# Performance work log

Hardware: AMD Instinct MI355X
Metric: run time of the kernel (lower is better)

Reference implementation:

```python
import jax, jax.numpy as jnp
import numpy as np

N = 50000          # total nodes
E = 800000         # edges (avg degree 16)
IN = 128           # in_feat
HID = 64           # hidden per head
HEADS = (4, 4, 1)
NEG_SLOPE = 0.2    # DGL GATConv leaky_relu default


def setup_inputs() -> dict:
    key = jax.random.key(0)
    ks = jax.random.split(key, 16)

    def w(k, shape, fan_in):
        return jax.random.normal(k, shape, jnp.float32) / np.float32(np.sqrt(fan_in))

    inp = {
        "feat": jax.random.normal(ks[0], (N, IN), jnp.float32),
        "src": jax.random.randint(ks[1], (E,), 0, N, jnp.int32),
        "dst": jax.random.randint(ks[2], (E,), 0, N, jnp.int32),
    }
    dims = [(IN, HEADS[0]), (HID * HEADS[0], HEADS[1]), (HID * HEADS[1], HEADS[2])]
    j = 3
    for i, (din, h) in enumerate(dims, 1):
        inp[f"W{i}"] = w(ks[j], (din, h * HID), din); j += 1
        inp[f"al{i}"] = w(ks[j], (h, HID), HID); j += 1
        inp[f"ar{i}"] = w(ks[j], (h, HID), HID); j += 1
        inp[f"b{i}"] = jnp.zeros((h * HID,), jnp.float32)
    return inp


def gat_layer(x, W, al, ar, b, src, dst, n_heads):
    # DGL GATConv: linear -> per-node attn logits -> edge leaky_relu ->
    # per-dst segment softmax -> weighted scatter-sum -> + bias
    h = (x @ W).reshape(N, n_heads, HID)                     # [N,H,D]
    el = jnp.einsum("nhd,hd->nh", h, al)                     # [N,H]
    er = jnp.einsum("nhd,hd->nh", h, ar)                     # [N,H]
    e = jax.nn.leaky_relu(el[src] + er[dst], NEG_SLOPE)      # [E,H]
    m = jax.ops.segment_max(e, dst, num_segments=N)          # [N,H]
    m = jnp.where(jnp.isfinite(m), m, 0.0)                   # empty segments -> -inf
    ex = jnp.exp(e - m[dst])                                 # [E,H]
    s = jax.ops.segment_sum(ex, dst, num_segments=N)         # [N,H]
    alpha = ex / s[dst]                                      # [E,H]
    msg = h[src] * alpha[:, :, None]                         # [E,H,D]
    out = jax.ops.segment_sum(msg, dst, num_segments=N)      # [N,H,D]
    return out + b.reshape(1, n_heads, HID)


def reference(feat, src, dst, W1, al1, ar1, b1, W2, al2, ar2, b2, W3, al3, ar3, b3):
    h = jax.nn.elu(gat_layer(feat, W1, al1, ar1, b1, src, dst, HEADS[0]))
    h = h.reshape(N, HEADS[0] * HID)                         # flatten heads
    h = jax.nn.elu(gat_layer(h, W2, al2, ar2, b2, src, dst, HEADS[1]))
    h = h.reshape(N, HEADS[1] * HID)
    h = gat_layer(h, W3, al3, ar3, b3, src, dst, HEADS[2])   # no activation
    return h.mean(axis=1)                                    # [N, HID]
```

## Files before the change

kernel.cpp:

```cpp
#include <hip/hip_runtime.h>
#include <math.h>

#define HID 64
#define NSLOPE 0.2f
#define SB 512
#define EXCAP 256

typedef __attribute__((ext_vector_type(8))) short short8v;
typedef __attribute__((ext_vector_type(4))) float float4v;

__device__ inline unsigned short f2bf(float x) {
  unsigned u = __float_as_uint(x);
  u += 0x7fffu + ((u >> 16) & 1u);
  return (unsigned short)(u >> 16);
}
__device__ inline float bf2f(unsigned short h) {
  return __uint_as_float(((unsigned)h) << 16);
}
__device__ inline float bflo(unsigned u) { return __uint_as_float(u << 16); }
__device__ inline float bfhi(unsigned u) { return __uint_as_float(u & 0xffff0000u); }

__global__ __launch_bounds__(256) void k_split(const float* __restrict__ x,
    unsigned short* __restrict__ hi, unsigned short* __restrict__ lo, int n) {
  int i = blockIdx.x * 256 + threadIdx.x;
  if (i < n) {
    float v = x[i];
    unsigned short h = f2bf(v);
    hi[i] = h;
    lo[i] = f2bf(v - bf2f(h));
  }
}

__global__ __launch_bounds__(256) void k_wsplit(const float* __restrict__ W,
    unsigned short* __restrict__ Whi, unsigned short* __restrict__ Wlo, int K, int N) {
  int i = blockIdx.x * 256 + threadIdx.x;
  if (i < N * K) {
    int n = i / K, k = i - n * K;
    float v = W[(size_t)k * N + n];
    unsigned short h = f2bf(v);
    Whi[i] = h;
    Wlo[i] = f2bf(v - bf2f(h));
  }
}

__global__ __launch_bounds__(256) void gemm_split(
    const unsigned short* __restrict__ Ahi, const unsigned short* __restrict__ Alo,
    const unsigned short* __restrict__ Bhi, const unsigned short* __restrict__ Blo,
    float* __restrict__ C, unsigned short* __restrict__ Gp, int M, int Nc, int K, int H) {
  __shared__ __align__(16) unsigned short AsHi[128 * 40];
  __shared__ __align__(16) unsigned short AsLo[128 * 40];
  __shared__ __align__(16) unsigned short BsHi[128 * 40];
  __shared__ __align__(16) unsigned short BsLo[128 * 40];
  const int tid = threadIdx.x;
  const int lane = tid & 63, wid = tid >> 6;
  const int wr = wid >> 1, wc = wid & 1;
  const int row0 = blockIdx.y * 128;
  const int col0 = blockIdx.x * 128;
  float4v acc[4][4];
  #pragma unroll
  for (int mi = 0; mi < 4; ++mi)
    #pragma unroll
    for (int ni = 0; ni < 4; ++ni)
      acc[mi][ni] = (float4v){0.f, 0.f, 0.f, 0.f};

  const int sr = tid >> 2;
  const int sc8 = (tid & 3) * 8;
  const int lr = lane & 15, lk = (lane >> 4) * 8;

  for (int k0 = 0; k0 < K; k0 += 32) {
    #pragma unroll
    for (int half = 0; half < 2; ++half) {
      int row = sr + half * 64;
      int arow = row0 + row; if (arow > M - 1) arow = M - 1;
      int brow = col0 + row; if (brow > Nc - 1) brow = Nc - 1;
      *(short8v*)&AsHi[row * 40 + sc8] = *(const short8v*)&Ahi[(size_t)arow * K + k0 + sc8];
      *(short8v*)&AsLo[row * 40 + sc8] = *(const short8v*)&Alo[(size_t)arow * K + k0 + sc8];
      *(short8v*)&BsHi[row * 40 + sc8] = *(const short8v*)&Bhi[(size_t)brow * K + k0 + sc8];
      *(short8v*)&BsLo[row * 40 + sc8] = *(const short8v*)&Blo[(size_t)brow * K + k0 + sc8];
    }
    __syncthreads();
    short8v ah[4], alv[4], bh[4], bl[4];
    #pragma unroll
    for (int mi = 0; mi < 4; ++mi) {
      int r = wr * 64 + mi * 16 + lr;
      ah[mi]  = *(const short8v*)&AsHi[r * 40 + lk];
      alv[mi] = *(const short8v*)&AsLo[r * 40 + lk];
    }
    #pragma unroll
    for (int ni = 0; ni < 4; ++ni) {
      int r = wc * 64 + ni * 16 + lr;
      bh[ni] = *(const short8v*)&BsHi[r * 40 + lk];
      bl[ni] = *(const short8v*)&BsLo[r * 40 + lk];
    }
    #pragma unroll
    for (int mi = 0; mi < 4; ++mi)
      #pragma unroll
      for (int ni = 0; ni < 4; ++ni) {
        acc[mi][ni] = __builtin_amdgcn_mfma_f32_16x16x32_bf16(ah[mi], bh[ni], acc[mi][ni], 0, 0, 0);
        acc[mi][ni] = __builtin_amdgcn_mfma_f32_16x16x32_bf16(ah[mi], bl[ni], acc[mi][ni], 0, 0, 0);
        acc[mi][ni] = __builtin_amdgcn_mfma_f32_16x16x32_bf16(alv[mi], bh[ni], acc[mi][ni], 0, 0, 0);
      }
    __syncthreads();
  }
  #pragma unroll
  for (int mi = 0; mi < 4; ++mi) {
    int rbase = row0 + wr * 64 + mi * 16 + (lane >> 4) * 4;
    #pragma unroll
    for (int ni = 0; ni < 4; ++ni) {
      int cc = col0 + wc * 64 + ni * 16 + (lane & 15);
      if (cc < Nc) {
        int gcol = (cc & 63) * H + (cc >> 6);
        #pragma unroll
        for (int q = 0; q < 4; ++q) {
          int rr = rbase + q;
          if (rr < M) {
            float v = acc[mi][ni][q];
            C[(size_t)rr * Nc + cc] = v;
            Gp[(size_t)rr * Nc + gcol] = f2bf(v);
          }
        }
      }
    }
  }
}

__global__ __launch_bounds__(256) void elr_kernel(const float* __restrict__ h,
    const float* __restrict__ al, const float* __restrict__ ar,
    float* __restrict__ el, float* __restrict__ er, int H, int N) {
  int n = blockIdx.x * 4 + (threadIdx.x >> 6);
  int lane = threadIdx.x & 63;
  if (n >= N) return;
  const float* hr = h + (size_t)n * H * HID;
  for (int hh = 0; hh < H; ++hh) {
    float v = hr[hh * HID + lane];
    float a = v * al[hh * HID + lane];
    float b = v * ar[hh * HID + lane];
    #pragma unroll
    for (int o = 32; o > 0; o >>= 1) { a += __shfl_xor(a, o); b += __shfl_xor(b, o); }
    if (lane == 0) { el[n * H + hh] = a; er[n * H + hh] = b; }
  }
}

__global__ void k_count(const int* __restrict__ dst, int* __restrict__ deg, int E) {
  int e = blockIdx.x * blockDim.x + threadIdx.x;
  if (e < E) atomicAdd(&deg[dst[e]], 1);
}
__global__ __launch_bounds__(SB) void k_blocksums(const int* __restrict__ deg,
                                                  int* __restrict__ bsums, int n) {
  __shared__ int s[SB];
  int t = threadIdx.x, i = blockIdx.x * SB + t;
  s[t] = (i < n) ? deg[i] : 0;
  __syncthreads();
  for (int o = SB >> 1; o > 0; o >>= 1) { if (t < o) s[t] += s[t + o]; __syncthreads(); }
  if (t == 0) bsums[blockIdx.x] = s[0];
}
__global__ __launch_bounds__(SB) void k_scancarry(const int* __restrict__ bsums,
                                                   int* __restrict__ carry, int nb) {
  __shared__ int s[SB];
  int t = threadIdx.x;
  int v = (t < nb) ? bsums[t] : 0;
  s[t] = v; __syncthreads();
  for (int o = 1; o < SB; o <<= 1) {
    int u = (t >= o) ? s[t - o] : 0;
    __syncthreads(); s[t] += u; __syncthreads();
  }
  if (t < nb) carry[t] = s[t] - v;
}
__global__ __launch_bounds__(SB) void k_offsets(const int* __restrict__ deg,
    const int* __restrict__ carry, int* __restrict__ offs, int n, int E) {
  __shared__ int s[SB];
  int t = threadIdx.x, i = blockIdx.x * SB + t;
  int v = (i < n) ? deg[i] : 0;
  s[t] = v; __syncthreads();
  for (int o = 1; o < SB; o <<= 1) {
    int u = (t >= o) ? s[t - o] : 0;
    __syncthreads(); s[t] += u; __syncthreads();
  }
  if (i < n) offs[i] = carry[blockIdx.x] + s[t] - v;
  if (i == n) offs[n] = E;
}
__global__ void k_fill(const int* __restrict__ src, const int* __restrict__ dst,
                       const int* __restrict__ offs, int* __restrict__ cursor,
                       int* __restrict__ esrc, int E) {
  int e = blockIdx.x * blockDim.x + threadIdx.x;
  if (e < E) {
    int d = dst[e];
    int slot = offs[d] + atomicAdd(&cursor[d], 1);
    esrc[slot] = src[e];
  }
}

template<int H, bool DO_ELU, bool SPLITOUT>
__global__ __launch_bounds__(64) void agg_kernel(const unsigned short* __restrict__ gp,
    const float* __restrict__ el, const float* __restrict__ er,
    const int* __restrict__ offs, const int* __restrict__ esrc,
    const float* __restrict__ bias,
    unsigned short* __restrict__ outHi, unsigned short* __restrict__ outLo,
    float* __restrict__ outF, int N) {
  constexpr int LPN = (H == 4) ? 32 : 16;
  constexpr int NPW = 64 / LPN;
  __shared__ __align__(16) float exs_all[NPW][EXCAP * H];
  const int lane = threadIdx.x;
  const int grp = lane / LPN;
  const int sl = lane % LPN;
  const int n = blockIdx.x * NPW + grp;
  if (n >= N) return;
  float* exs = exs_all[grp];
  const int off = offs[n];
  const int deg = offs[n + 1] - off;
  float ern[H];
  if (H == 4) {
    float4 R = *(const float4*)&er[n * 4];
    ern[0] = R.x; ern[1] = R.y; ern[2] = R.z; ern[3] = R.w;
  } else {
    ern[0] = er[n];
  }
  float sum[H];
  #pragma unroll
  for (int h = 0; h < H; ++h) sum[h] = 0.f;
  for (int base = 0; base < deg; base += LPN) {
    int i = base + sl;
    if (i < deg) {
      int s = esrc[off + i];
      if (H == 4) {
        float4 L = *(const float4*)&el[s * 4];
        float lv[4] = {L.x, L.y, L.z, L.w};
        float exv[4];
        #pragma unroll
        for (int h = 0; h < 4; ++h) {
          float e = lv[h] + ern[h];
          e = e > 0.f ? e : NSLOPE * e;
          exv[h] = __expf(fminf(e, 80.f));
          sum[h] += exv[h];
        }
        if (i < EXCAP)
          *(float4*)&exs[i * 4] = make_float4(exv[0], exv[1], exv[2], exv[3]);
      } else {
        float e = el[s] + ern[0];
        e = e > 0.f ? e : NSLOPE * e;
        float x = __expf(fminf(e, 80.f));
        sum[0] += x;
        if (i < EXCAP) exs[i] = x;
      }
    }
  }
  float inv[H];
  #pragma unroll
  for (int h = 0; h < H; ++h) {
    float v = sum[h];
    #pragma unroll
    for (int o = LPN / 2; o > 0; o >>= 1) v += __shfl_xor(v, o);
    inv[h] = v > 0.f ? 1.f / v : 0.f;
  }
  asm volatile("s_waitcnt lgkmcnt(0)" ::: "memory");
  const int degc = deg < EXCAP ? deg : EXCAP;
  int t = 0;
  if (H == 4) {
    float acc[8];
    #pragma unroll
    for (int k = 0; k < 8; ++k) acc[k] = 0.f;
    for (; t + 4 <= degc; t += 4) {
      int4 sa = *(const int4*)&esrc[off + t];
      int s[4] = {sa.x, sa.y, sa.z, sa.w};
      uint4 g[4];
      #pragma unroll
      for (int j = 0; j < 4; ++j)
        g[j] = *(const uint4*)&gp[(size_t)s[j] * 256 + sl * 8];
      #pragma unroll
      for (int j = 0; j < 4; ++j) {
        float4 x = *(const float4*)&exs[(t + j) * 4];
        acc[0] = fmaf(bflo(g[j].x), x.x, acc[0]);
        acc[1] = fmaf(bfhi(g[j].x), x.y, acc[1]);
        acc[2] = fmaf(bflo(g[j].y), x.z, acc[2]);
        acc[3] = fmaf(bfhi(g[j].y), x.w, acc[3]);
        acc[4] = fmaf(bflo(g[j].z), x.x, acc[4]);
        acc[5] = fmaf(bfhi(g[j].z), x.y, acc[5]);
        acc[6] = fmaf(bflo(g[j].w), x.z, acc[6]);
        acc[7] = fmaf(bfhi(g[j].w), x.w, acc[7]);
      }
    }
    for (; t < degc; ++t) {
      int s = esrc[off + t];
      uint4 g = *(const uint4*)&gp[(size_t)s * 256 + sl * 8];
      float4 x = *(const float4*)&exs[t * 4];
      acc[0] = fmaf(bflo(g.x), x.x, acc[0]);
      acc[1] = fmaf(bfhi(g.x), x.y, acc[1]);
      acc[2] = fmaf(bflo(g.y), x.z, acc[2]);
      acc[3] = fmaf(bfhi(g.y), x.w, acc[3]);
      acc[4] = fmaf(bflo(g.z), x.x, acc[4]);
      acc[5] = fmaf(bfhi(g.z), x.y, acc[5]);
      acc[6] = fmaf(bflo(g.w), x.z, acc[6]);
      acc[7] = fmaf(bfhi(g.w), x.w, acc[7]);
    }
    for (; t < deg; ++t) {
      int s = esrc[off + t];
      float4 L = *(const float4*)&el[s * 4];
      float lv[4] = {L.x, L.y, L.z, L.w};
      float xv[4];
      #pragma unroll
      for (int h = 0; h < 4; ++h) {
        float e = lv[h] + ern[h];
        e = e > 0.f ? e : NSLOPE * e;
        xv[h] = __expf(fminf(e, 80.f));
      }
      uint4 g = *(const uint4*)&gp[(size_t)s * 256 + sl * 8];
      acc[0] = fmaf(bflo(g.x), xv[0], acc[0]);
      acc[1] = fmaf(bfhi(g.x), xv[1], acc[1]);
      acc[2] = fmaf(bflo(g.y), xv[2], acc[2]);
      acc[3] = fmaf(bfhi(g.y), xv[3], acc[3]);
      acc[4] = fmaf(bflo(g.z), xv[0], acc[4]);
      acc[5] = fmaf(bfhi(g.z), xv[1], acc[5]);
      acc[6] = fmaf(bflo(g.w), xv[2], acc[6]);
      acc[7] = fmaf(bfhi(g.w), xv[3], acc[7]);
    }
    #pragma unroll
    for (int dd = 0; dd < 2; ++dd) {
      int d = 2 * sl + dd;
      #pragma unroll
      for (int hh = 0; hh < 4; ++hh) {
        float v = fmaf(acc[dd * 4 + hh], inv[hh], bias[hh * HID + d]);
        if (DO_ELU) v = v > 0.f ? v : expm1f(v);
        size_t oi = (size_t)n * 256 + hh * HID + d;
        if (SPLITOUT) {
          unsigned short hb = f2bf(v);
          outHi[oi] = hb;
          outLo[oi] = f2bf(v - bf2f(hb));
        } else {
          outF[oi] = v;
        }
      }
    }
  } else {
    float acc[4];
    #pragma unroll
    for (int k = 0; k < 4; ++k) acc[k] = 0.f;
    for (; t + 8 <= degc; t += 8) {
      int4 sa = *(const int4*)&esrc[off + t];
      int4 sb = *(const int4*)&esrc[off + t + 4];
      int s[8] = {sa.x, sa.y, sa.z, sa.w, sb.x, sb.y, sb.z, sb.w};
      uint2 g[8];
      #pragma unroll
      for (int j = 0; j < 8; ++j)
        g[j] = *(const uint2*)&gp[(size_t)s[j] * 64 + sl * 4];
      #pragma unroll
      for (int j = 0; j < 8; ++j) {
        float x = exs[t + j];
        acc[0] = fmaf(bflo(g[j].x), x, acc[0]);
        acc[1] = fmaf(bfhi(g[j].x), x, acc[1]);
        acc[2] = fmaf(bflo(g[j].y), x, acc[2]);
        acc[3] = fmaf(bfhi(g[j].y), x, acc[3]);
      }
    }
    for (; t < degc; ++t) {
      int s = esrc[off + t];
      uint2 g = *(const uint2*)&gp[(size_t)s * 64 + sl * 4];
      float x = exs[t];
      acc[0] = fmaf(bflo(g.x), x, acc[0]);
      acc[1] = fmaf(bfhi(g.x), x, acc[1]);
      acc[2] = fmaf(bflo(g.y), x, acc[2]);
      acc[3] = fmaf(bfhi(g.y), x, acc[3]);
    }
    for (; t < deg; ++t) {
      int s = esrc[off + t];
      float e = el[s] + ern[0];
      e = e > 0.f ? e : NSLOPE * e;
      float x = __expf(fminf(e, 80.f));
      uint2 g = *(const uint2*)&gp[(size_t)s * 64 + sl * 4];
      acc[0] = fmaf(bflo(g.x), x, acc[0]);
      acc[1] = fmaf(bfhi(g.x), x, acc[1]);
      acc[2] = fmaf(bflo(g.y), x, acc[2]);
      acc[3] = fmaf(bfhi(g.y), x, acc[3]);
    }
    #pragma unroll
    for (int k = 0; k < 4; ++k) {
      int d = 4 * sl + k;
      float v = fmaf(acc[k], inv[0], bias[d]);
      if (DO_ELU) v = v > 0.f ? v : expm1f(v);
      size_t oi = (size_t)n * HID + d;
      if (SPLITOUT) {
        unsigned short hb = f2bf(v);
        outHi[oi] = hb;
        outLo[oi] = f2bf(v - bf2f(hb));
      } else {
        outF[oi] = v;
      }
    }
  }
}

extern "C" void kernel_launch(void* const* d_in, const int* in_sizes, int n_in,
                              void* d_out, int out_size, void* d_ws, size_t ws_size,
                              hipStream_t stream) {
  const float* feat = (const float*)d_in[0];
  const int* src = (const int*)d_in[1];
  const int* dst = (const int*)d_in[2];
  const float* W1 = (const float*)d_in[3];
  const float* al1 = (const float*)d_in[4];
  const float* ar1 = (const float*)d_in[5];
  const float* b1 = (const float*)d_in[6];
  const float* W2 = (const float*)d_in[7];
  const float* al2 = (const float*)d_in[8];
  const float* ar2 = (const float*)d_in[9];
  const float* b2 = (const float*)d_in[10];
  const float* W3 = (const float*)d_in[11];
  const float* al3 = (const float*)d_in[12];
  const float* ar3 = (const float*)d_in[13];
  const float* b3 = (const float*)d_in[14];
  const int N = in_sizes[0] / 128;
  const int E = in_sizes[1];

  char* w = (char*)d_ws;
  auto alloc = [&](size_t bytes) {
    void* p = (void*)w;
    w += (bytes + 255) & ~(size_t)255;
    return p;
  };
  unsigned short* pHi = (unsigned short*)alloc((size_t)N * 256 * 2);
  unsigned short* pLo = (unsigned short*)alloc((size_t)N * 256 * 2);
  float* Cbuf = (float*)alloc((size_t)N * 256 * 4);
  unsigned short* Gp = (unsigned short*)alloc((size_t)N * 256 * 2);
  float* el = (float*)alloc((size_t)N * 4 * 4);
  float* er = (float*)alloc((size_t)N * 4 * 4);
  int* deg = (int*)alloc((size_t)N * 4);
  int* cursor = (int*)alloc((size_t)N * 4);
  int* offs = (int*)alloc((size_t)(N + 1) * 4);
  int nb = (N + SB - 1) / SB;
  int* bsums = (int*)alloc((size_t)nb * 4);
  int* carry = (int*)alloc((size_t)nb * 4);
  int* esrc = (int*)alloc((size_t)E * 4);
  unsigned short* W1h = (unsigned short*)alloc((size_t)256 * 128 * 2);
  unsigned short* W1l = (unsigned short*)alloc((size_t)256 * 128 * 2);
  unsigned short* W2h = (unsigned short*)alloc((size_t)256 * 256 * 2);
  unsigned short* W2l = (unsigned short*)alloc((size_t)256 * 256 * 2);
  unsigned short* W3h = (unsigned short*)alloc((size_t)64 * 256 * 2);
  unsigned short* W3l = (unsigned short*)alloc((size_t)64 * 256 * 2);

  hipMemsetAsync(deg, 0, (size_t)N * 4, stream);
  hipMemsetAsync(cursor, 0, (size_t)N * 4, stream);
  int eb = (E + 255) / 256;
  k_count<<<eb, 256, 0, stream>>>(dst, deg, E);
  k_blocksums<<<nb, SB, 0, stream>>>(deg, bsums, N);
  k_scancarry<<<1, SB, 0, stream>>>(bsums, carry, nb);
  k_offsets<<<nb, SB, 0, stream>>>(deg, carry, offs, N, E);
  k_fill<<<eb, 256, 0, stream>>>(src, dst, offs, cursor, esrc, E);

  k_wsplit<<<(256 * 128 + 255) / 256, 256, 0, stream>>>(W1, W1h, W1l, 128, 256);
  k_wsplit<<<(256 * 256 + 255) / 256, 256, 0, stream>>>(W2, W2h, W2l, 256, 256);
  k_wsplit<<<(64 * 256 + 255) / 256, 256, 0, stream>>>(W3, W3h, W3l, 256, 64);

  k_split<<<((N * 128) + 255) / 256, 256, 0, stream>>>(feat, pHi, pLo, N * 128);

  int rg = (N + 127) / 128;
  int ng4 = (N + 3) / 4;
  int ag4 = (N + 1) / 2;
  int ag1 = (N + 3) / 4;
  gemm_split<<<dim3(2, rg), 256, 0, stream>>>(pHi, pLo, W1h, W1l, Cbuf, Gp, N, 256, 128, 4);
  elr_kernel<<<ng4, 256, 0, stream>>>(Cbuf, al1, ar1, el, er, 4, N);
  agg_kernel<4, true, true><<<ag4, 64, 0, stream>>>(Gp, el, er, offs, esrc, b1, pHi, pLo, nullptr, N);
  gemm_split<<<dim3(2, rg), 256, 0, stream>>>(pHi, pLo, W2h, W2l, Cbuf, Gp, N, 256, 256, 4);
  elr_kernel<<<ng4, 256, 0, stream>>>(Cbuf, al2, ar2, el, er, 4, N);
  agg_kernel<4, true, true><<<ag4, 64, 0, stream>>>(Gp, el, er, offs, esrc, b2, pHi, pLo, nullptr, N);
  gemm_split<<<dim3(1, rg), 256, 0, stream>>>(pHi, pLo, W3h, W3l, Cbuf, Gp, N, 64, 256, 1);
  elr_kernel<<<ng4, 256, 0, stream>>>(Cbuf, al3, ar3, el, er, 1, N);
  agg_kernel<1, false, false><<<ag1, 64, 0, stream>>>(Gp, el, er, offs, esrc, b3, nullptr, nullptr, (float*)d_out, N);
}
```

Baseline: 456.7 us.

## Fuse attention logit computation into GEMM epilogue and sort CSR neighbor lists

Drops the fp32 C buffer write and the separate elr kernel. The GEMM epilogue now computes per-head el/er partial dot products with lane shuffles and accumulates them into zeroed buffers with atomicAdd, which cuts about 50MB of fp32 traffic per layer. A new k_sort kernel sorts each destination's source list (for degree 64 or less) so gathers in aggregation hit memory more locally. The trade-off is extra memsets, atomics and a per-node sort launch, and float atomics make the summation order nondeterministic.

```diff
diff --git a/kernel.cpp b/kernel.cpp
--- a/kernel.cpp
+++ b/kernel.cpp
@@ -46,7 +46,10 @@
 __global__ __launch_bounds__(256) void gemm_split(
     const unsigned short* __restrict__ Ahi, const unsigned short* __restrict__ Alo,
     const unsigned short* __restrict__ Bhi, const unsigned short* __restrict__ Blo,
-    float* __restrict__ C, unsigned short* __restrict__ Gp, int M, int Nc, int K, int H) {
+    unsigned short* __restrict__ Gp,
+    const float* __restrict__ al, const float* __restrict__ ar,
+    float* __restrict__ el, float* __restrict__ er,
+    int M, int Nc, int K, int H) {
   __shared__ __align__(16) unsigned short AsHi[128 * 40];
   __shared__ __align__(16) unsigned short AsLo[128 * 40];
   __shared__ __align__(16) unsigned short BsHi[128 * 40];
@@ -79,12 +82,12 @@
       *(short8v*)&BsLo[row * 40 + sc8] = *(const short8v*)&Blo[(size_t)brow * K + k0 + sc8];
     }
     __syncthreads();
-    short8v ah[4], alv[4], bh[4], bl[4];
+    short8v ah[4], alv_[4], bh[4], bl[4];
     #pragma unroll
     for (int mi = 0; mi < 4; ++mi) {
       int r = wr * 64 + mi * 16 + lr;
-      ah[mi]  = *(const short8v*)&AsHi[r * 40 + lk];
-      alv[mi] = *(const short8v*)&AsLo[r * 40 + lk];
+      ah[mi]   = *(const short8v*)&AsHi[r * 40 + lk];
+      alv_[mi] = *(const short8v*)&AsLo[r * 40 + lk];
     }
     #pragma unroll
     for (int ni = 0; ni < 4; ++ni) {
@@ -98,9 +101,22 @@
       for (int ni = 0; ni < 4; ++ni) {
         acc[mi][ni] = __builtin_amdgcn_mfma_f32_16x16x32_bf16(ah[mi], bh[ni], acc[mi][ni], 0, 0, 0);
         acc[mi][ni] = __builtin_amdgcn_mfma_f32_16x16x32_bf16(ah[mi], bl[ni], acc[mi][ni], 0, 0, 0);
-        acc[mi][ni] = __builtin_amdgcn_mfma_f32_16x16x32_bf16(alv[mi], bh[ni], acc[mi][ni], 0, 0, 0);
+        acc[mi][ni] = __builtin_amdgcn_mfma_f32_16x16x32_bf16(alv_[mi], bh[ni], acc[mi][ni], 0, 0, 0);
       }
     __syncthreads();
+  }
+  float aco[4], arco[4];
+  int hhv[4];
+  #pragma unroll
+  for (int ni = 0; ni < 4; ++ni) {
+    int cc = col0 + wc * 64 + ni * 16 + (lane & 15);
+    if (cc < Nc) {
+      hhv[ni] = cc >> 6;
+      aco[ni] = al[hhv[ni] * HID + (cc & 63)];
+      arco[ni] = ar[hhv[ni] * HID + (cc & 63)];
+    } else {
+      hhv[ni] = 0; aco[ni] = 0.f; arco[ni] = 0.f;
+    }
   }
   #pragma unroll
   for (int mi = 0; mi < 4; ++mi) {
@@ -108,36 +124,27 @@
     #pragma unroll
     for (int ni = 0; ni < 4; ++ni) {
       int cc = col0 + wc * 64 + ni * 16 + (lane & 15);
-      if (cc < Nc) {
+      bool fragvalid = (col0 + wc * 64 + ni * 16) < Nc;
+      if (fragvalid) {
         int gcol = (cc & 63) * H + (cc >> 6);
         #pragma unroll
         for (int q = 0; q < 4; ++q) {
           int rr = rbase + q;
-          if (rr < M) {
-            float v = acc[mi][ni][q];
-            C[(size_t)rr * Nc + cc] = v;
-            Gp[(size_t)rr * Nc + gcol] = f2bf(v);
+          float v = acc[mi][ni][q];
+          if (rr < M) Gp[(size_t)rr * Nc + gcol] = f2bf(v);
+          float pel = v * aco[ni], per_ = v * arco[ni];
+          #pragma unroll
+          for (int o = 1; o < 16; o <<= 1) {
+            pel += __shfl_xor(pel, o);
+            per_ += __shfl_xor(per_, o);
+          }
+          if ((lane & 15) == 0 && rr < M) {
+            atomicAdd(&el[rr * H + hhv[ni]], pel);
+            atomicAdd(&er[rr * H + hhv[ni]], per_);
           }
         }
       }
     }
-  }
-}
-
-__global__ __launch_bounds__(256) void elr_kernel(const float* __restrict__ h,
-    const float* __restrict__ al, const float* __restrict__ ar,
-    float* __restrict__ el, float* __restrict__ er, int H, int N) {
-  int n = blockIdx.x * 4 + (threadIdx.x >> 6);
-  int lane = threadIdx.x & 63;
-  if (n >= N) return;
-  const float* hr = h + (size_t)n * H * HID;
-  for (int hh = 0; hh < H; ++hh) {
-    float v = hr[hh * HID + lane];
-    float a = v * al[hh * HID + lane];
-    float b = v * ar[hh * HID + lane];
-    #pragma unroll
-    for (int o = 32; o > 0; o >>= 1) { a += __shfl_xor(a, o); b += __shfl_xor(b, o); }
-    if (lane == 0) { el[n * H + hh] = a; er[n * H + hh] = b; }
   }
 }
 
@@ -188,6 +195,19 @@
     int slot = offs[d] + atomicAdd(&cursor[d], 1);
     esrc[slot] = src[e];
   }
+}
+__global__ __launch_bounds__(64) void k_sort(const int* __restrict__ offs,
+                                             int* __restrict__ esrc, int N) {
+  int n = blockIdx.x, lane = threadIdx.x;
+  int off = offs[n], deg = offs[n + 1] - off;
+  if (deg <= 1 || deg > 64) return;
+  int key = (lane < deg) ? esrc[off + lane] : 0x7fffffff;
+  int rank = 0;
+  for (int j = 0; j < deg; ++j) {
+    int kj = __shfl(key, j);
+    rank += (kj < key) || (kj == key && j < lane);
+  }
+  if (lane < deg) esrc[off + rank] = key;
 }
 
 template<int H, bool DO_ELU, bool SPLITOUT>
@@ -417,10 +437,10 @@
   };
   unsigned short* pHi = (unsigned short*)alloc((size_t)N * 256 * 2);
   unsigned short* pLo = (unsigned short*)alloc((size_t)N * 256 * 2);
-  float* Cbuf = (float*)alloc((size_t)N * 256 * 4);
   unsigned short* Gp = (unsigned short*)alloc((size_t)N * 256 * 2);
-  float* el = (float*)alloc((size_t)N * 4 * 4);
-  float* er = (float*)alloc((size_t)N * 4 * 4);
+  float* elr = (float*)alloc((size_t)2 * N * 4 * 4);
+  float* el = elr;
+  float* er = elr + (size_t)N * 4;
   int* deg = (int*)alloc((size_t)N * 4);
   int* cursor = (int*)alloc((size_t)N * 4);
   int* offs = (int*)alloc((size_t)(N + 1) * 4);
@@ -443,6 +463,7 @@
   k_scancarry<<<1, SB, 0, stream>>>(bsums, carry, nb);
   k_offsets<<<nb, SB, 0, stream>>>(deg, carry, offs, N, E);
   k_fill<<<eb, 256, 0, stream>>>(src, dst, offs, cursor, esrc, E);
+  k_sort<<<N, 64, 0, stream>>>(offs, esrc, N);
 
   k_wsplit<<<(256 * 128 + 255) / 256, 256, 0, stream>>>(W1, W1h, W1l, 128, 256);
   k_wsplit<<<(256 * 256 + 255) / 256, 256, 0, stream>>>(W2, W2h, W2l, 256, 256);
@@ -451,16 +472,16 @@
   k_split<<<((N * 128) + 255) / 256, 256, 0, stream>>>(feat, pHi, pLo, N * 128);
 
   int rg = (N + 127) / 128;
-  int ng4 = (N + 3) / 4;
   int ag4 = (N + 1) / 2;
   int ag1 = (N + 3) / 4;
-  gemm_split<<<dim3(2, rg), 256, 0, stream>>>(pHi, pLo, W1h, W1l, Cbuf, Gp, N, 256, 128, 4);
-  elr_kernel<<<ng4, 256, 0, stream>>>(Cbuf, al1, ar1, el, er, 4, N);
+  size_t elrBytes = (size_t)2 * N * 4 * 4;
+  hipMemsetAsync(elr, 0, elrBytes, stream);
+  gemm_split<<<dim3(2, rg), 256, 0, stream>>>(pHi, pLo, W1h, W1l, Gp, al1, ar1, el, er, N, 256, 128, 4);
   agg_kernel<4, true, true><<<ag4, 64, 0, stream>>>(Gp, el, er, offs, esrc, b1, pHi, pLo, nullptr, N);
-  gemm_split<<<dim3(2, rg), 256, 0, stream>>>(pHi, pLo, W2h, W2l, Cbuf, Gp, N, 256, 256, 4);
-  elr_kernel<<<ng4, 256, 0, stream>>>(Cbuf, al2, ar2, el, er, 4, N);
+  hipMemsetAsync(elr, 0, elrBytes, stream);
+  gemm_split<<<dim3(2, rg), 256, 0, stream>>>(pHi, pLo, W2h, W2l, Gp, al2, ar2, el, er, N, 256, 256, 4);
   agg_kernel<4, true, true><<<ag4, 64, 0, stream>>>(Gp, el, er, offs, esrc, b2, pHi, pLo, nullptr, N);
-  gemm_split<<<dim3(1, rg), 256, 0, stream>>>(pHi, pLo, W3h, W3l, Cbuf, Gp, N, 64, 256, 1);
-  elr_kernel<<<ng4, 256, 0, stream>>>(Cbuf, al3, ar3, el, er, 1, N);
+  hipMemsetAsync(elr, 0, elrBytes, stream);
+  gemm_split<<<dim3(1, rg), 256, 0, stream>>>(pHi, pLo, W3h, W3l, Gp, al3, ar3, el, er, N, 64, 256, 1);
   agg_kernel<1, false, false><<<ag1, 64, 0, stream>>>(Gp, el, er, offs, esrc, b3, nullptr, nullptr, (float*)d_out, N);
 }
```

After: 578.5 us. 26.7% more time.

## Bin edges by destination block before scattering into CSR source array

Applied to the files above, without the earlier changes.

The single-pass CSR fill is replaced by two passes. The first appends packed (dst,src) pairs into per-256-node buckets using a per-bucket counter, falling back to the direct path on overflow. The second pass has one block per bucket perform the per-node atomic slot claim and esrc write. The goal is to make the per-node atomics and esrc writes localized instead of scattered across the whole array. In exchange it adds an extra buffer round trip, heavily contended atomics on the few bucket counters, and a 16-bit packing that assumes node ids below 65536.

```diff
diff --git a/kernel.cpp b/kernel.cpp
--- a/kernel.cpp
+++ b/kernel.cpp
@@ -5,6 +5,7 @@
 #define NSLOPE 0.2f
 #define SB 512
 #define EXCAP 256
+#define BCAP 8192
 
 typedef __attribute__((ext_vector_type(8))) short short8v;
 typedef __attribute__((ext_vector_type(4))) float float4v;
@@ -179,14 +180,32 @@
   if (i < n) offs[i] = carry[blockIdx.x] + s[t] - v;
   if (i == n) offs[n] = E;
 }
-__global__ void k_fill(const int* __restrict__ src, const int* __restrict__ dst,
+__global__ void k_binA(const int* __restrict__ src, const int* __restrict__ dst,
+                       int* __restrict__ bcur, unsigned* __restrict__ bbuf,
                        const int* __restrict__ offs, int* __restrict__ cursor,
                        int* __restrict__ esrc, int E) {
-  int e = blockIdx.x * blockDim.x + threadIdx.x;
-  if (e < E) {
-    int d = dst[e];
+  int e = blockIdx.x * 256 + threadIdx.x;
+  if (e >= E) return;
+  int d = dst[e], s = src[e];
+  int b = d >> 8;
+  int pos = atomicAdd(&bcur[b], 1);
+  if (pos < BCAP) {
+    bbuf[(size_t)b * BCAP + pos] = ((unsigned)d << 16) | (unsigned)s;
+  } else {
     int slot = offs[d] + atomicAdd(&cursor[d], 1);
-    esrc[slot] = src[e];
+    esrc[slot] = s;
+  }
+}
+__global__ __launch_bounds__(256) void k_binB(const int* __restrict__ bcur,
+    const unsigned* __restrict__ bbuf, const int* __restrict__ offs,
+    int* __restrict__ cursor, int* __restrict__ esrc) {
+  int b = blockIdx.x;
+  int cnt = bcur[b]; if (cnt > BCAP) cnt = BCAP;
+  for (int i = threadIdx.x; i < cnt; i += 256) {
+    unsigned v = bbuf[(size_t)b * BCAP + i];
+    int d = (int)(v >> 16), s = (int)(v & 0xffffu);
+    int slot = offs[d] + atomicAdd(&cursor[d], 1);
+    esrc[slot] = s;
   }
 }
 
@@ -428,6 +447,9 @@
   int* bsums = (int*)alloc((size_t)nb * 4);
   int* carry = (int*)alloc((size_t)nb * 4);
   int* esrc = (int*)alloc((size_t)E * 4);
+  int nbk = (N + 255) >> 8;
+  int* bcur = (int*)alloc((size_t)nbk * 4);
+  unsigned* bbuf = (unsigned*)alloc((size_t)nbk * BCAP * 4);
   unsigned short* W1h = (unsigned short*)alloc((size_t)256 * 128 * 2);
   unsigned short* W1l = (unsigned short*)alloc((size_t)256 * 128 * 2);
   unsigned short* W2h = (unsigned short*)alloc((size_t)256 * 256 * 2);
@@ -437,12 +459,14 @@
 
   hipMemsetAsync(deg, 0, (size_t)N * 4, stream);
   hipMemsetAsync(cursor, 0, (size_t)N * 4, stream);
+  hipMemsetAsync(bcur, 0, (size_t)nbk * 4, stream);
   int eb = (E + 255) / 256;
   k_count<<<eb, 256, 0, stream>>>(dst, deg, E);
   k_blocksums<<<nb, SB, 0, stream>>>(deg, bsums, N);
   k_scancarry<<<1, SB, 0, stream>>>(bsums, carry, nb);
   k_offsets<<<nb, SB, 0, stream>>>(deg, carry, offs, N, E);
-  k_fill<<<eb, 256, 0, stream>>>(src, dst, offs, cursor, esrc, E);
+  k_binA<<<eb, 256, 0, stream>>>(src, dst, bcur, bbuf, offs, cursor, esrc, E);
+  k_binB<<<nbk, 256, 0, stream>>>(bcur, bbuf, offs, cursor, esrc);
 
   k_wsplit<<<(256 * 128 + 255) / 256, 256, 0, stream>>>(W1, W1h, W1l, 128, 256);
   k_wsplit<<<(256 * 256 + 255) / 256, 256, 0, stream>>>(W2, W2h, W2l, 256, 256);
```

New measurement: 887.0 us. 94.2% more time.
